# Performance work log

Hardware: AMD Instinct MI355X
Metric: run time of the kernel (lower is better)

## Reference

```python
import jax, jax.numpy as jnp
import numpy as np

B, L0, L1, C, HC = 16, 1024, 3136, 768, 8


def setup_inputs() -> dict:
    key = jax.random.key(0)
    ks = jax.random.split(key, 9)
    x = jax.random.normal(ks[0], (B, L0 + L1, C), dtype=jnp.float32)
    # 1x1 convs == per-token linear layers; store weights as [in, out]
    s_in = 1.0 / np.sqrt(C)
    s_hc = 1.0 / np.sqrt(HC)
    W00 = jax.random.normal(ks[1], (C, HC), dtype=jnp.float32) * s_in
    b00 = jnp.zeros((HC,), dtype=jnp.float32)
    W01 = jax.random.normal(ks[2], (C, HC), dtype=jnp.float32) * s_in
    b01 = jnp.zeros((HC,), dtype=jnp.float32)
    W1 = jax.random.normal(ks[3], (HC, C), dtype=jnp.float32) * s_hc
    b1 = jnp.zeros((C,), dtype=jnp.float32)
    W2 = jax.random.normal(ks[4], (HC, C), dtype=jnp.float32) * s_hc
    b2 = jnp.zeros((C,), dtype=jnp.float32)
    return {"x": x, "W00": W00, "b00": b00, "W01": W01, "b01": b01,
            "W1": W1, "b1": b1, "W2": W2, "b2": b2, "size": L0}


def _fovea(t):
    # torch Fovea on feature map [B,D,H,W] flattens to [B,D,H*W] and
    # softmaxes over spatial positions; in token layout [B,L,D] that is
    # a softmax over the token axis per channel, then elementwise mul.
    return jax.nn.softmax(t, axis=1) * t


def reference(x, W00, b00, W01, b01, W1, b1, W2, b2, size):
    x0 = x[:, :size, :]          # [B, L0, C] template tokens
    x1 = x[:, size:, :]          # [B, L1, C] search tokens
    x0t = x0 @ W00 + b00         # [B, L0, HC]  (1x1 conv0_0)
    x1t = x1 @ W01 + b01         # [B, L1, HC]  (1x1 conv0_1)

    # bidirectional UNSCALED cross-attention (no 1/sqrt(d) factor)
    a01 = jax.nn.softmax(jnp.einsum('bld,bmd->blm', x0t, x1t), axis=-1)  # [B,L0,L1]
    x0_1 = jnp.einsum('blm,bmd->bld', a01, x1t)                          # [B,L0,HC]
    a10 = jax.nn.softmax(jnp.einsum('bmd,bld->bml', x1t, x0t), axis=-1)  # [B,L1,L0]
    x1_0 = jnp.einsum('bml,bld->bmd', a10, x0t)                          # [B,L1,HC]

    x0o = _fovea(x0t) + x0_1     # fovea(x0) + x0_1
    x1o = _fovea(x1_0) + x1t     # fovea(x1_0) + x1

    y0 = x0o @ W1 + b1           # [B, L0, C]  (conv1x1)
    y1 = x1o @ W2 + b2           # [B, L1, C]  (conv1x1_2)

    # token2feature: [B,L,C] -> [B,C,H,W] with H=W=sqrt(L)
    Bn = x.shape[0]
    H0 = int(round(size ** 0.5))
    H1 = int(round((x.shape[1] - size) ** 0.5))
    f0 = jnp.transpose(y0, (0, 2, 1)).reshape(Bn, -1, H0, H0)
    f1 = jnp.transpose(y1, (0, 2, 1)).reshape(Bn, -1, H1, H1)
    return (f0, f1)
```

## Files before the change

kernel.cpp:

```cpp
#include <hip/hip_runtime.h>

#define NB 16
#define CIN 768
#define HC 8
#define LT 4160
#define LOG2E 1.44269504088896f

__global__ __launch_bounds__(256) void proj_kernel(
    const float* __restrict__ x,
    const float* __restrict__ W00, const float* __restrict__ b00,
    const float* __restrict__ W01, const float* __restrict__ b01,
    float* __restrict__ x0t, float* __restrict__ x1t)
{
  const int tid  = threadIdx.x;
  const int lane = tid & 63;
  const int wid  = tid >> 6;
  const int b    = blockIdx.y;
  int bx = blockIdx.x;

  const float* W; const float* bias; float* out; int segoff, Lseg;
  if (bx < 16) { W = W00; bias = b00; out = x0t; segoff = 0;    Lseg = 1024; }
  else { bx -= 16; W = W01; bias = b01; out = x1t; segoff = 1024; Lseg = 3136; }

  float wreg[3][4][8];
#pragma unroll
  for (int k = 0; k < 3; ++k) {
#pragma unroll
    for (int j = 0; j < 4; ++j) {
      const int c = lane * 4 + j + 256 * k;
      const float4 a  = *reinterpret_cast<const float4*>(W + (size_t)c * 8);
      const float4 d4 = *reinterpret_cast<const float4*>(W + (size_t)c * 8 + 4);
      wreg[k][j][0]=a.x;  wreg[k][j][1]=a.y;  wreg[k][j][2]=a.z;  wreg[k][j][3]=a.w;
      wreg[k][j][4]=d4.x; wreg[k][j][5]=d4.y; wreg[k][j][6]=d4.z; wreg[k][j][7]=d4.w;
    }
  }
  const float bv = (lane < 8) ? bias[lane] : 0.f;

  const int l0 = bx * 64 + wid * 16;
  const float* xb = x + ((size_t)b * LT + segoff) * CIN;
  float* ob = out + (size_t)b * Lseg * HC;

  for (int r = 0; r < 16; ++r) {
    const int l = l0 + r;
    const float* xr = xb + (size_t)l * CIN;
    float acc[8] = {0.f,0.f,0.f,0.f,0.f,0.f,0.f,0.f};
#pragma unroll
    for (int k = 0; k < 3; ++k) {
      const float4 xv = *reinterpret_cast<const float4*>(xr + lane * 4 + 256 * k);
      const float xs[4] = {xv.x, xv.y, xv.z, xv.w};
#pragma unroll
      for (int j = 0; j < 4; ++j)
#pragma unroll
        for (int d = 0; d < 8; ++d) acc[d] = fmaf(xs[j], wreg[k][j][d], acc[d]);
    }
#pragma unroll
    for (int off = 1; off < 8; off <<= 1)
#pragma unroll
      for (int d = 0; d < 8; ++d) acc[d] += __shfl_xor(acc[d], off, 64);
    const int d7 = lane & 7;
    float v = acc[0];
#pragma unroll
    for (int d = 1; d < 8; ++d) v = (d7 == d) ? acc[d] : v;
#pragma unroll
    for (int off = 8; off < 64; off <<= 1) v += __shfl_xor(v, off, 64);
    if (lane < 8) ob[(size_t)l * HC + lane] = v + bv;
  }
}

__global__ __launch_bounds__(512) void attn_kernel(
    const float* __restrict__ x0t, const float* __restrict__ x1t,
    float* __restrict__ x0_1, float* __restrict__ x1_0)
{
  __shared__ float kvs[8 * 1024];
  const int tid  = threadIdx.x;
  const int lane = tid & 63;
  const int wid  = tid >> 6;
  const int b    = blockIdx.y;
  int bx = blockIdx.x;

  const float *Q, *K; float* O; int Lq, Lk;
  if (bx < 32) { Q = x0t; K = x1t; O = x0_1; Lq = 1024; Lk = 3136; }
  else { bx -= 32; Q = x1t; K = x0t; O = x1_0; Lq = 3136; Lk = 1024; }

  const int q0 = bx * 32 + wid * 4;
  const float* Qb = Q + ((size_t)b * Lq + q0) * HC;
  float q[4][8];
#pragma unroll
  for (int r = 0; r < 4; ++r) {
    const float4 a = *reinterpret_cast<const float4*>(Qb + r * 8);
    const float4 c = *reinterpret_cast<const float4*>(Qb + r * 8 + 4);
    q[r][0]=a.x*LOG2E; q[r][1]=a.y*LOG2E; q[r][2]=a.z*LOG2E; q[r][3]=a.w*LOG2E;
    q[r][4]=c.x*LOG2E; q[r][5]=c.y*LOG2E; q[r][6]=c.z*LOG2E; q[r][7]=c.w*LOG2E;
  }
  float sum[4] = {0.f,0.f,0.f,0.f};
  float acc[4][8];
#pragma unroll
  for (int r = 0; r < 4; ++r)
#pragma unroll
    for (int d = 0; d < 8; ++d) acc[r][d] = 0.f;

  const float* Kb = K + (size_t)b * Lk * HC;

  for (int c0 = 0; c0 < Lk; c0 += 1024) {
    const int clen = min(1024, Lk - c0);
    __syncthreads();
    for (int j = tid; j < clen; j += 512) {
      const float* kr = Kb + (size_t)(c0 + j) * HC;
      const float4 a = *reinterpret_cast<const float4*>(kr);
      const float4 c = *reinterpret_cast<const float4*>(kr + 4);
      kvs[0*1024+j]=a.x; kvs[1*1024+j]=a.y; kvs[2*1024+j]=a.z; kvs[3*1024+j]=a.w;
      kvs[4*1024+j]=c.x; kvs[5*1024+j]=c.y; kvs[6*1024+j]=c.z; kvs[7*1024+j]=c.w;
    }
    __syncthreads();
    const int iters = clen >> 6;
#pragma unroll 2
    for (int it = 0; it < iters; ++it) {
      const int j = it * 64 + lane;
      float kx[8];
#pragma unroll
      for (int d = 0; d < 8; ++d) kx[d] = kvs[d * 1024 + j];
#pragma unroll
      for (int r = 0; r < 4; ++r) {
        float s = 0.f;
#pragma unroll
        for (int d = 0; d < 8; ++d) s = fmaf(q[r][d], kx[d], s);
        const float p = exp2f(s);
        sum[r] += p;
#pragma unroll
        for (int d = 0; d < 8; ++d) acc[r][d] = fmaf(p, kx[d], acc[r][d]);
      }
    }
  }

  const int d7 = lane & 7;
#pragma unroll
  for (int r = 0; r < 4; ++r) {
    float s = sum[r];
#pragma unroll
    for (int off = 1; off < 8; off <<= 1) {
      s += __shfl_xor(s, off, 64);
#pragma unroll
      for (int d = 0; d < 8; ++d) acc[r][d] += __shfl_xor(acc[r][d], off, 64);
    }
    float v = acc[r][0];
#pragma unroll
    for (int d = 1; d < 8; ++d) v = (d7 == d) ? acc[r][d] : v;
#pragma unroll
    for (int off = 8; off < 64; off <<= 1) {
      v += __shfl_xor(v, off, 64);
      s += __shfl_xor(s, off, 64);
    }
    if (lane < 8)
      O[((size_t)b * Lq + q0 + r) * HC + lane] = __fdividef(v, s);
  }
}

__global__ __launch_bounds__(256) void fovea_kernel(
    const float* __restrict__ x0t, const float* __restrict__ x0_1, float* __restrict__ x0o,
    const float* __restrict__ x1_0, const float* __restrict__ x1t, float* __restrict__ x1o)
{
  __shared__ float tv[3136];
  __shared__ float reds[4];
  int bid = blockIdx.x;
  const float *T, *A; float* O; int L;
  if (bid < 128) { T = x0t; A = x0_1; O = x0o; L = 1024; }
  else { bid -= 128; T = x1_0; A = x1t; O = x1o; L = 3136; }

  const int tid  = threadIdx.x;
  const int lane = tid & 63;
  const int wid  = tid >> 6;
  const int b = bid >> 3;
  const int d = bid & 7;
  const float* t = T + (size_t)b * L * HC + d;
  const float* a = A + (size_t)b * L * HC + d;
  float* o = O + (size_t)b * L * HC + d;

  float s = 0.f;
  for (int l = tid; l < L; l += 256) {
    const float v = t[(size_t)l * HC];
    tv[l] = v;
    s += __expf(v);
  }
#pragma unroll
  for (int off = 32; off > 0; off >>= 1) s += __shfl_xor(s, off, 64);
  if (lane == 0) reds[wid] = s;
  __syncthreads();
  const float inv = 1.f / (reds[0] + reds[1] + reds[2] + reds[3]);

  for (int l = tid; l < L; l += 256) {
    const float v = tv[l];
    o[(size_t)l * HC] = __expf(v) * inv * v + a[(size_t)l * HC];
  }
}

__global__ __launch_bounds__(256) void outproj_kernel(
    const float* __restrict__ x0o, const float* __restrict__ W1, const float* __restrict__ b1,
    const float* __restrict__ x1o, const float* __restrict__ W2, const float* __restrict__ b2,
    float* __restrict__ out)
{
  const int tx = threadIdx.x;
  const int ty = threadIdx.y;
  const int b  = blockIdx.z;
  const int c0 = blockIdx.y * 16;
  int bx = blockIdx.x;

  const float *XO, *W, *bias; float* ob; int L, nj;
  if (bx < 4) { XO = x0o; W = W1; bias = b1; ob = out; L = 1024; nj = 4; }
  else { bx -= 4; XO = x1o; W = W2; bias = b2;
         ob = out + (size_t)NB * CIN * 1024; L = 3136; nj = 7; }

  const int l0 = bx * (nj * 64);

  float w[4][8], bv[4];
#pragma unroll
  for (int k = 0; k < 4; ++k) {
    const int c = c0 + ty * 4 + k;
#pragma unroll
    for (int d = 0; d < 8; ++d) w[k][d] = W[d * CIN + c];
    bv[k] = bias[c];
  }

  for (int j = 0; j < nj; ++j) {
    const int l = l0 + j * 64 + tx;
    const float* xr = XO + ((size_t)b * L + l) * HC;
    const float4 a  = *reinterpret_cast<const float4*>(xr);
    const float4 c4 = *reinterpret_cast<const float4*>(xr + 4);
    const float qv[8] = {a.x, a.y, a.z, a.w, c4.x, c4.y, c4.z, c4.w};
#pragma unroll
    for (int k = 0; k < 4; ++k) {
      float acc = bv[k];
#pragma unroll
      for (int d = 0; d < 8; ++d) acc = fmaf(qv[d], w[k][d], acc);
      ob[((size_t)b * CIN + (c0 + ty * 4 + k)) * L + l] = acc;
    }
  }
}

extern "C" void kernel_launch(void* const* d_in, const int* in_sizes, int n_in,
                              void* d_out, int out_size, void* d_ws, size_t ws_size,
                              hipStream_t stream)
{
  const float* x   = (const float*)d_in[0];
  const float* W00 = (const float*)d_in[1];
  const float* b00 = (const float*)d_in[2];
  const float* W01 = (const float*)d_in[3];
  const float* b01 = (const float*)d_in[4];
  const float* W1  = (const float*)d_in[5];
  const float* b1  = (const float*)d_in[6];
  const float* W2  = (const float*)d_in[7];
  const float* b2  = (const float*)d_in[8];
  float* out = (float*)d_out;

  float* ws   = (float*)d_ws;
  float* x0t  = ws;
  float* x1t  = x0t  + (size_t)16*1024*8;
  float* x0_1 = x1t  + (size_t)16*3136*8;
  float* x1_0 = x0_1 + (size_t)16*1024*8;
  float* x0o  = x1_0 + (size_t)16*3136*8;
  float* x1o  = x0o  + (size_t)16*1024*8;

  proj_kernel<<<dim3(65, 16), 256, 0, stream>>>(x, W00, b00, W01, b01, x0t, x1t);
  attn_kernel<<<dim3(130, 16), 512, 0, stream>>>(x0t, x1t, x0_1, x1_0);
  fovea_kernel<<<256, 256, 0, stream>>>(x0t, x0_1, x0o, x1_0, x1t, x1o);
  outproj_kernel<<<dim3(11, 48, 16), dim3(64, 4), 0, stream>>>(
      x0o, W1, b1, x1o, W2, b2, out);
}
```

Measured before the change: 486.1 us.

## Fuse fovea softmax sums into producers, read K from global, prefetch rows

The fovea column-softmax denominators are now accumulated with atomics in the projection and attention kernels that produce the data, so the fovea kernel becomes a coalesced elementwise pass over float4 rows instead of a strided per-channel reduction. The attention kernel drops its LDS staging and barriers and reads K directly from global memory with register prefetch, using smaller 256-thread blocks and twice as many of them. The projection and output-projection loops also software-prefetch the next row. This adds an extra memset and atomics, and exp values are summed without max subtraction as before.

```diff
diff --git a/kernel.cpp b/kernel.cpp
--- a/kernel.cpp
+++ b/kernel.cpp
@@ -10,16 +10,19 @@
     const float* __restrict__ x,
     const float* __restrict__ W00, const float* __restrict__ b00,
     const float* __restrict__ W01, const float* __restrict__ b01,
-    float* __restrict__ x0t, float* __restrict__ x1t)
-{
+    float* __restrict__ x0t, float* __restrict__ x1t,
+    float* __restrict__ S0)
+{
+  __shared__ float pred[4][8];
   const int tid  = threadIdx.x;
   const int lane = tid & 63;
   const int wid  = tid >> 6;
   const int b    = blockIdx.y;
   int bx = blockIdx.x;
 
+  const bool seg0 = (bx < 16);
   const float* W; const float* bias; float* out; int segoff, Lseg;
-  if (bx < 16) { W = W00; bias = b00; out = x0t; segoff = 0;    Lseg = 1024; }
+  if (seg0) { W = W00; bias = b00; out = x0t; segoff = 0;    Lseg = 1024; }
   else { bx -= 16; W = W01; bias = b01; out = x1t; segoff = 1024; Lseg = 3136; }
 
   float wreg[3][4][8];
@@ -40,14 +43,25 @@
   const float* xb = x + ((size_t)b * LT + segoff) * CIN;
   float* ob = out + (size_t)b * Lseg * HC;
 
+  float4 xv[3];
+#pragma unroll
+  for (int k = 0; k < 3; ++k)
+    xv[k] = *reinterpret_cast<const float4*>(xb + (size_t)l0 * CIN + lane * 4 + 256 * k);
+
+  float es = 0.f;
   for (int r = 0; r < 16; ++r) {
     const int l = l0 + r;
-    const float* xr = xb + (size_t)l * CIN;
+    const float4 cur[3] = {xv[0], xv[1], xv[2]};
+    if (r < 15) {
+      const float* xr = xb + (size_t)(l + 1) * CIN;
+#pragma unroll
+      for (int k = 0; k < 3; ++k)
+        xv[k] = *reinterpret_cast<const float4*>(xr + lane * 4 + 256 * k);
+    }
     float acc[8] = {0.f,0.f,0.f,0.f,0.f,0.f,0.f,0.f};
 #pragma unroll
     for (int k = 0; k < 3; ++k) {
-      const float4 xv = *reinterpret_cast<const float4*>(xr + lane * 4 + 256 * k);
-      const float xs[4] = {xv.x, xv.y, xv.z, xv.w};
+      const float xs[4] = {cur[k].x, cur[k].y, cur[k].z, cur[k].w};
 #pragma unroll
       for (int j = 0; j < 4; ++j)
 #pragma unroll
@@ -63,26 +77,39 @@
     for (int d = 1; d < 8; ++d) v = (d7 == d) ? acc[d] : v;
 #pragma unroll
     for (int off = 8; off < 64; off <<= 1) v += __shfl_xor(v, off, 64);
-    if (lane < 8) ob[(size_t)l * HC + lane] = v + bv;
-  }
-}
-
-__global__ __launch_bounds__(512) void attn_kernel(
+    if (lane < 8) {
+      const float val = v + bv;
+      ob[(size_t)l * HC + lane] = val;
+      if (seg0) es += __expf(val);
+    }
+  }
+
+  if (seg0) {
+    if (lane < 8) pred[wid][lane] = es;
+    __syncthreads();
+    if (tid < 8)
+      atomicAdd(&S0[(size_t)b * 8 + tid],
+                pred[0][tid] + pred[1][tid] + pred[2][tid] + pred[3][tid]);
+  }
+}
+
+__global__ __launch_bounds__(256) void attn_kernel(
     const float* __restrict__ x0t, const float* __restrict__ x1t,
-    float* __restrict__ x0_1, float* __restrict__ x1_0)
-{
-  __shared__ float kvs[8 * 1024];
+    float* __restrict__ x0_1, float* __restrict__ x1_0,
+    float* __restrict__ S1)
+{
+  __shared__ float sred[4][8];
   const int tid  = threadIdx.x;
   const int lane = tid & 63;
   const int wid  = tid >> 6;
   const int b    = blockIdx.y;
   int bx = blockIdx.x;
 
-  const float *Q, *K; float* O; int Lq, Lk;
-  if (bx < 32) { Q = x0t; K = x1t; O = x0_1; Lq = 1024; Lk = 3136; }
-  else { bx -= 32; Q = x1t; K = x0t; O = x1_0; Lq = 3136; Lk = 1024; }
-
-  const int q0 = bx * 32 + wid * 4;
+  const float *Q, *K; float* O; int Lq, Lk; bool a2;
+  if (bx < 64) { Q = x0t; K = x1t; O = x0_1; Lq = 1024; Lk = 3136; a2 = false; }
+  else { bx -= 64; Q = x1t; K = x0t; O = x1_0; Lq = 3136; Lk = 1024; a2 = true; }
+
+  const int q0 = bx * 16 + wid * 4;
   const float* Qb = Q + ((size_t)b * Lq + q0) * HC;
   float q[4][8];
 #pragma unroll
@@ -100,39 +127,32 @@
     for (int d = 0; d < 8; ++d) acc[r][d] = 0.f;
 
   const float* Kb = K + (size_t)b * Lk * HC;
-
-  for (int c0 = 0; c0 < Lk; c0 += 1024) {
-    const int clen = min(1024, Lk - c0);
-    __syncthreads();
-    for (int j = tid; j < clen; j += 512) {
-      const float* kr = Kb + (size_t)(c0 + j) * HC;
-      const float4 a = *reinterpret_cast<const float4*>(kr);
-      const float4 c = *reinterpret_cast<const float4*>(kr + 4);
-      kvs[0*1024+j]=a.x; kvs[1*1024+j]=a.y; kvs[2*1024+j]=a.z; kvs[3*1024+j]=a.w;
-      kvs[4*1024+j]=c.x; kvs[5*1024+j]=c.y; kvs[6*1024+j]=c.z; kvs[7*1024+j]=c.w;
-    }
-    __syncthreads();
-    const int iters = clen >> 6;
-#pragma unroll 2
-    for (int it = 0; it < iters; ++it) {
-      const int j = it * 64 + lane;
-      float kx[8];
-#pragma unroll
-      for (int d = 0; d < 8; ++d) kx[d] = kvs[d * 1024 + j];
-#pragma unroll
-      for (int r = 0; r < 4; ++r) {
-        float s = 0.f;
-#pragma unroll
-        for (int d = 0; d < 8; ++d) s = fmaf(q[r][d], kx[d], s);
-        const float p = exp2f(s);
-        sum[r] += p;
-#pragma unroll
-        for (int d = 0; d < 8; ++d) acc[r][d] = fmaf(p, kx[d], acc[r][d]);
-      }
+  const int iters = Lk >> 6;
+
+  float4 pa = *reinterpret_cast<const float4*>(Kb + (size_t)lane * 8);
+  float4 pc = *reinterpret_cast<const float4*>(Kb + (size_t)lane * 8 + 4);
+
+  for (int it = 0; it < iters; ++it) {
+    const float kx[8] = {pa.x, pa.y, pa.z, pa.w, pc.x, pc.y, pc.z, pc.w};
+    if (it + 1 < iters) {
+      const float* kr = Kb + (size_t)((it + 1) * 64 + lane) * 8;
+      pa = *reinterpret_cast<const float4*>(kr);
+      pc = *reinterpret_cast<const float4*>(kr + 4);
+    }
+#pragma unroll
+    for (int r = 0; r < 4; ++r) {
+      float s = 0.f;
+#pragma unroll
+      for (int d = 0; d < 8; ++d) s = fmaf(q[r][d], kx[d], s);
+      const float p = exp2f(s);
+      sum[r] += p;
+#pragma unroll
+      for (int d = 0; d < 8; ++d) acc[r][d] = fmaf(p, kx[d], acc[r][d]);
     }
   }
 
   const int d7 = lane & 7;
+  float es = 0.f;
 #pragma unroll
   for (int r = 0; r < 4; ++r) {
     float s = sum[r];
@@ -150,47 +170,56 @@
       v += __shfl_xor(v, off, 64);
       s += __shfl_xor(s, off, 64);
     }
-    if (lane < 8)
-      O[((size_t)b * Lq + q0 + r) * HC + lane] = __fdividef(v, s);
+    if (lane < 8) {
+      const float val = __fdividef(v, s);
+      O[((size_t)b * Lq + q0 + r) * HC + lane] = val;
+      if (a2) es += __expf(val);
+    }
+  }
+
+  if (a2) {
+    if (lane < 8) sred[wid][lane] = es;
+    __syncthreads();
+    if (tid < 8)
+      atomicAdd(&S1[(size_t)b * 8 + tid],
+                sred[0][tid] + sred[1][tid] + sred[2][tid] + sred[3][tid]);
   }
 }
 
 __global__ __launch_bounds__(256) void fovea_kernel(
     const float* __restrict__ x0t, const float* __restrict__ x0_1, float* __restrict__ x0o,
-    const float* __restrict__ x1_0, const float* __restrict__ x1t, float* __restrict__ x1o)
-{
-  __shared__ float tv[3136];
-  __shared__ float reds[4];
-  int bid = blockIdx.x;
-  const float *T, *A; float* O; int L;
-  if (bid < 128) { T = x0t; A = x0_1; O = x0o; L = 1024; }
-  else { bid -= 128; T = x1_0; A = x1t; O = x1o; L = 3136; }
-
-  const int tid  = threadIdx.x;
-  const int lane = tid & 63;
-  const int wid  = tid >> 6;
-  const int b = bid >> 3;
-  const int d = bid & 7;
-  const float* t = T + (size_t)b * L * HC + d;
-  const float* a = A + (size_t)b * L * HC + d;
-  float* o = O + (size_t)b * L * HC + d;
-
-  float s = 0.f;
-  for (int l = tid; l < L; l += 256) {
-    const float v = t[(size_t)l * HC];
-    tv[l] = v;
-    s += __expf(v);
-  }
-#pragma unroll
-  for (int off = 32; off > 0; off >>= 1) s += __shfl_xor(s, off, 64);
-  if (lane == 0) reds[wid] = s;
-  __syncthreads();
-  const float inv = 1.f / (reds[0] + reds[1] + reds[2] + reds[3]);
-
-  for (int l = tid; l < L; l += 256) {
-    const float v = tv[l];
-    o[(size_t)l * HC] = __expf(v) * inv * v + a[(size_t)l * HC];
-  }
+    const float* __restrict__ x1_0, const float* __restrict__ x1t, float* __restrict__ x1o,
+    const float* __restrict__ S0, const float* __restrict__ S1)
+{
+  const int b = blockIdx.y;
+  int bx = blockIdx.x;
+  const float *T, *A, *S; float* O; int L;
+  if (bx < 4) { T = x0t; A = x0_1; O = x0o; S = S0; L = 1024; }
+  else { bx -= 4; T = x1_0; A = x1t; O = x1o; S = S1; L = 3136; }
+
+  const int l = bx * 256 + threadIdx.x;
+  if (l >= L) return;
+
+  float inv[8];
+#pragma unroll
+  for (int d = 0; d < 8; ++d) inv[d] = 1.f / S[(size_t)b * 8 + d];
+
+  const size_t base = ((size_t)b * L + l) * HC;
+  const float4 ta = *reinterpret_cast<const float4*>(T + base);
+  const float4 tc = *reinterpret_cast<const float4*>(T + base + 4);
+  const float4 aa = *reinterpret_cast<const float4*>(A + base);
+  const float4 ac = *reinterpret_cast<const float4*>(A + base + 4);
+  float4 oa, oc;
+  oa.x = __expf(ta.x) * inv[0] * ta.x + aa.x;
+  oa.y = __expf(ta.y) * inv[1] * ta.y + aa.y;
+  oa.z = __expf(ta.z) * inv[2] * ta.z + aa.z;
+  oa.w = __expf(ta.w) * inv[3] * ta.w + aa.w;
+  oc.x = __expf(tc.x) * inv[4] * tc.x + ac.x;
+  oc.y = __expf(tc.y) * inv[5] * tc.y + ac.y;
+  oc.z = __expf(tc.z) * inv[6] * tc.z + ac.z;
+  oc.w = __expf(tc.w) * inv[7] * tc.w + ac.w;
+  *reinterpret_cast<float4*>(O + base)     = oa;
+  *reinterpret_cast<float4*>(O + base + 4) = oc;
 }
 
 __global__ __launch_bounds__(256) void outproj_kernel(
@@ -220,12 +249,18 @@
     bv[k] = bias[c];
   }
 
+  const float* xr0 = XO + ((size_t)b * L + l0 + tx) * HC;
+  float4 a  = *reinterpret_cast<const float4*>(xr0);
+  float4 c4 = *reinterpret_cast<const float4*>(xr0 + 4);
+
   for (int j = 0; j < nj; ++j) {
     const int l = l0 + j * 64 + tx;
-    const float* xr = XO + ((size_t)b * L + l) * HC;
-    const float4 a  = *reinterpret_cast<const float4*>(xr);
-    const float4 c4 = *reinterpret_cast<const float4*>(xr + 4);
     const float qv[8] = {a.x, a.y, a.z, a.w, c4.x, c4.y, c4.z, c4.w};
+    if (j + 1 < nj) {
+      const float* xr = XO + ((size_t)b * L + l + 64) * HC;
+      a  = *reinterpret_cast<const float4*>(xr);
+      c4 = *reinterpret_cast<const float4*>(xr + 4);
+    }
 #pragma unroll
     for (int k = 0; k < 4; ++k) {
       float acc = bv[k];
@@ -258,10 +293,17 @@
   float* x1_0 = x0_1 + (size_t)16*1024*8;
   float* x0o  = x1_0 + (size_t)16*3136*8;
   float* x1o  = x0o  + (size_t)16*1024*8;
-
-  proj_kernel<<<dim3(65, 16), 256, 0, stream>>>(x, W00, b00, W01, b01, x0t, x1t);
-  attn_kernel<<<dim3(130, 16), 512, 0, stream>>>(x0t, x1t, x0_1, x1_0);
-  fovea_kernel<<<256, 256, 0, stream>>>(x0t, x0_1, x0o, x1_0, x1t, x1o);
+  float* S0   = x1o  + (size_t)16*3136*8;
+  float* S1   = S0 + 128;
+
+  hipMemsetAsync(S0, 0, 256 * sizeof(float), stream);
+
+  proj_kernel<<<dim3(65, 16), 256, 0, stream>>>(
+      x, W00, b00, W01, b01, x0t, x1t, S0);
+  attn_kernel<<<dim3(260, 16), 256, 0, stream>>>(
+      x0t, x1t, x0_1, x1_0, S1);
+  fovea_kernel<<<dim3(17, 16), 256, 0, stream>>>(
+      x0t, x0_1, x0o, x1_0, x1t, x1o, S0, S1);
   outproj_kernel<<<dim3(11, 48, 16), dim3(64, 4), 0, stream>>>(
       x0o, W1, b1, x1o, W2, b2, out);
 }
```

Result: faster. 470.2 us (-3.3%).
